# Kernel optimization log

Measured on AMD Instinct MI355X. Metric: run time of the kernel, lower is better.

The kernel has to match this reference:

```python
import jax, jax.numpy as jnp
import numpy as np

H = 8  # pinyin_feature_size = embedding_dim = GRU hidden size
VOCAB = 27


def setup_inputs() -> dict:
    key = jax.random.key(0)
    ks = jax.random.split(key, 10)
    B, T = 131072, 24
    inputs = jax.random.randint(ks[0], (B, T), 0, VOCAB, dtype=jnp.int32)
    emb = jax.random.normal(ks[1], (VOCAB, H), dtype=jnp.float32)
    emb = emb.at[0].set(0.0)  # padding_idx=0
    s = 0.25  # ~ 1/sqrt(hidden) init scale like torch GRU
    w_ih1 = jax.random.normal(ks[2], (3 * H, H), dtype=jnp.float32) * s
    w_hh1 = jax.random.normal(ks[3], (3 * H, H), dtype=jnp.float32) * s
    b_ih1 = jax.random.normal(ks[4], (3 * H,), dtype=jnp.float32) * s
    b_hh1 = jax.random.normal(ks[5], (3 * H,), dtype=jnp.float32) * s
    w_ih2 = jax.random.normal(ks[6], (3 * H, H), dtype=jnp.float32) * s
    w_hh2 = jax.random.normal(ks[7], (3 * H, H), dtype=jnp.float32) * s
    b_ih2 = jax.random.normal(ks[8], (3 * H,), dtype=jnp.float32) * s
    b_hh2 = jax.random.normal(ks[9], (3 * H,), dtype=jnp.float32) * s
    return {"inputs": inputs, "emb": emb,
            "w_ih1": w_ih1, "w_hh1": w_hh1, "b_ih1": b_ih1, "b_hh1": b_hh1,
            "w_ih2": w_ih2, "w_hh2": w_hh2, "b_ih2": b_ih2, "b_hh2": b_hh2}


def _gru_layer(x_seq, w_ih, w_hh, b_ih, b_hh):
    # x_seq: [B, T, H_in] -> all hidden states [B, T, H], final h [B, H]
    B = x_seq.shape[0]
    # precompute input-side gates for all timesteps: [T, B, 3H]
    gi_all = jnp.einsum('bti,gi->tbg', x_seq, w_ih) + b_ih
    h0 = jnp.zeros((B, H), dtype=x_seq.dtype)

    def cell(h, gi):
        gh = h @ w_hh.T + b_hh  # [B, 3H]
        i_r, i_z, i_n = jnp.split(gi, 3, axis=-1)
        h_r, h_z, h_n = jnp.split(gh, 3, axis=-1)
        r = jax.nn.sigmoid(i_r + h_r)
        z = jax.nn.sigmoid(i_z + h_z)
        n = jnp.tanh(i_n + r * h_n)
        h_new = (1.0 - z) * n + z * h
        return h_new, h_new

    h_last, hs = jax.lax.scan(cell, h0, gi_all)
    return jnp.swapaxes(hs, 0, 1), h_last  # [B, T, H], [B, H]


def reference(inputs, emb, w_ih1, w_hh1, b_ih1, b_hh1,
              w_ih2, w_hh2, b_ih2, b_hh2):
    # padding_idx=0 => row 0 of the table is zero
    emb_eff = emb.at[0].set(0.0)
    x = emb_eff[inputs]  # [B, T, H]
    h1_seq, _ = _gru_layer(x, w_ih1, w_hh1, b_ih1, b_hh1)
    # dropout(0.15) between layers is inactive in eval mode
    _, h2_last = _gru_layer(h1_seq, w_ih2, w_hh2, b_ih2, b_hh2)
    return h2_last  # [B, H] == output[1][-1]
```

## Files before the change

kernel.cpp:

```cpp
#include <hip/hip_runtime.h>


typedef __fp16 h2f    __attribute__((ext_vector_type(2)));
typedef __fp16 half8  __attribute__((ext_vector_type(8)));
typedef float  f32x16 __attribute__((ext_vector_type(16)));

#define LOG2E 1.44269504088896f

__device__ __forceinline__ h2f pk2f(float a, float b) {
  return __builtin_amdgcn_cvt_pkrtz(a, b);
}

union H8U { half8 h; unsigned u[4]; h2f p[4]; };

__device__ __forceinline__ unsigned from_upper(unsigned x) {
  auto r = __builtin_amdgcn_permlane32_swap((int)x, (int)x, false, false);
  return (unsigned)r[1];
}

__global__ __launch_bounds__(256, 4) void gru2_mfma(
    const int* __restrict__ inputs,
    const float* __restrict__ emb,
    const float* __restrict__ w_ih1, const float* __restrict__ w_hh1,
    const float* __restrict__ b_ih1, const float* __restrict__ b_hh1,
    const float* __restrict__ w_ih2, const float* __restrict__ w_hh2,
    const float* __restrict__ b_ih2, const float* __restrict__ b_hh2,
    float* __restrict__ out)
{
  __shared__ float G1f[27 * 33];
  __shared__ int   TK[128 * 25];

  const int tid   = threadIdx.x;
  const int lane  = tid & 63;
  const int wid   = tid >> 6;
  const int half_ = lane >> 5;
  const int col   = lane & 31;

  for (int idx = tid; idx < 27 * 24; idx += 256) {
    const int tok = idx / 24, g = idx - tok * 24;
    const float s = (g < 16) ? -LOG2E : 2.f * LOG2E;
    float a = b_ih1[g] + ((g < 16) ? b_hh1[g] : 0.f);
    if (tok != 0) {
      #pragma unroll
      for (int j = 0; j < 8; ++j) a = fmaf(w_ih1[g * 8 + j], emb[tok * 8 + j], a);
    }
    G1f[tok * 33 + g] = s * a;
  }

  const long gbase = (long)blockIdx.x * (128 * 24);
  #pragma unroll
  for (int k = 0; k < 12; ++k) {
    const int i = tid + k * 256;
    TK[(i / 24) * 25 + (i % 24)] = inputs[gbase + i];
  }
  __syncthreads();

  const int sl = wid * 32 + col;
  unsigned pkw[4] = {0u, 0u, 0u, 0u};
  #pragma unroll
  for (int t = 0; t < 24; ++t)
    pkw[t / 6] |= ((unsigned)TK[sl * 25 + t]) << (5 * (t % 6));
  const unsigned pk0 = pkw[0], pk1 = pkw[1], pk2_ = pkw[2], pk3 = pkw[3];

  auto tok_at = [&](int t) -> unsigned {
    const unsigned pw = (t < 6) ? pk0 : (t < 12) ? pk1 : (t < 18) ? pk2_ : pk3;
    return (pw >> (5 * (t % 6))) & 31u;
  };

  auto loadW = [&](const float* w) -> half8 {
    H8U u;
    u.u[0] = u.u[1] = u.u[2] = u.u[3] = 0u;
    if (half_ == 0 && col < 24) {
      const float s = (col < 16) ? -LOG2E : 2.f * LOG2E;
      const float4* p = (const float4*)(w + col * 8);
      const float4 x = p[0], y = p[1];
      u.p[0] = pk2f(x.x * s, x.y * s);
      u.p[1] = pk2f(x.z * s, x.w * s);
      u.p[2] = pk2f(y.x * s, y.y * s);
      u.p[3] = pk2f(y.z * s, y.w * s);
    }
    return u.h;
  };
  const half8 wa1  = loadW(w_hh1);
  const half8 wa2i = loadW(w_ih2);
  const half8 wa2h = loadW(w_hh2);

  f32x16 c2;
  #pragma unroll
  for (int r = 0; r < 16; ++r) {
    const int m = (r & 3) + 8 * (r >> 2) + 4 * half_;
    float v;
    if (m < 16)      v = -LOG2E * (b_ih2[m] + b_hh2[m]);
    else if (m < 24) v = 2.f * LOG2E * b_hh2[m];
    else             v = 0.f;
    c2[r] = v;
  }
  float bn1[4], bi2n[4];
  #pragma unroll
  for (int i = 0; i < 4; ++i) {
    bn1[i]  = 2.f * LOG2E * b_hh1[16 + 4 * half_ + i];
    bi2n[i] = 2.f * LOG2E * b_ih2[16 + 4 * half_ + i];
  }

  float h1v[4] = {0.f, 0.f, 0.f, 0.f}, h2v[4] = {0.f, 0.f, 0.f, 0.f};
  H8U f1, f2;
  f1.u[0] = f1.u[1] = f1.u[2] = f1.u[3] = 0u;
  f2 = f1;

  const float* g1base = G1f + half_ * 4;

  f32x16 c1;
  c1[8] = bn1[0]; c1[9] = bn1[1]; c1[10] = bn1[2]; c1[11] = bn1[3];
  c1[12] = 0.f; c1[13] = 0.f; c1[14] = 0.f; c1[15] = 0.f;
  float gin1[4];
  {
    const float* gp = g1base + tok_at(0) * 33;
    c1[0] = gp[0];  c1[1] = gp[1];  c1[2] = gp[2];  c1[3] = gp[3];
    c1[4] = gp[8];  c1[5] = gp[9];  c1[6] = gp[10]; c1[7] = gp[11];
    gin1[0] = gp[16]; gin1[1] = gp[17]; gin1[2] = gp[18]; gin1[3] = gp[19];
  }
  f32x16 d1 = c1;

  #pragma unroll
  for (int t = 0; t < 24; ++t) {
    float nc[8], ng[4];
    if (t < 23) {
      const float* gp = g1base + tok_at(t + 1) * 33;
      nc[0] = gp[0];  nc[1] = gp[1];  nc[2] = gp[2];  nc[3] = gp[3];
      nc[4] = gp[8];  nc[5] = gp[9];  nc[6] = gp[10]; nc[7] = gp[11];
      ng[0] = gp[16]; ng[1] = gp[17]; ng[2] = gp[18]; ng[3] = gp[19];
    }

    const f32x16 dh = __builtin_amdgcn_mfma_f32_32x32x16_f16(wa2h, f2.h, c2, 0, 0, 0);

    #pragma unroll
    for (int i = 0; i < 4; ++i) {
      const float r = __builtin_amdgcn_rcpf(1.f + __builtin_amdgcn_exp2f(d1[i]));
      const float z = __builtin_amdgcn_rcpf(1.f + __builtin_amdgcn_exp2f(d1[4 + i]));
      const float na = fmaf(r, d1[8 + i], gin1[i]);
      const float n = fmaf(-2.f, __builtin_amdgcn_rcpf(1.f + __builtin_amdgcn_exp2f(na)), 1.f);
      h1v[i] = n + z * (h1v[i] - n);
    }
    {
      const unsigned a = __builtin_bit_cast(unsigned, pk2f(h1v[0], h1v[1]));
      const unsigned b = __builtin_bit_cast(unsigned, pk2f(h1v[2], h1v[3]));
      f1.u[0] = a; f1.u[1] = b;
      f1.u[2] = from_upper(a); f1.u[3] = from_upper(b);
    }

    const f32x16 dg = __builtin_amdgcn_mfma_f32_32x32x16_f16(wa2i, f1.h, dh, 0, 0, 0);

    if (t < 23) {
      c1[0] = nc[0]; c1[1] = nc[1]; c1[2] = nc[2]; c1[3] = nc[3];
      c1[4] = nc[4]; c1[5] = nc[5]; c1[6] = nc[6]; c1[7] = nc[7];
      gin1[0] = ng[0]; gin1[1] = ng[1]; gin1[2] = ng[2]; gin1[3] = ng[3];
      d1 = __builtin_amdgcn_mfma_f32_32x32x16_f16(wa1, f1.h, c1, 0, 0, 0);
    }

    #pragma unroll
    for (int i = 0; i < 4; ++i) {
      const float r = __builtin_amdgcn_rcpf(1.f + __builtin_amdgcn_exp2f(dg[i]));
      const float z = __builtin_amdgcn_rcpf(1.f + __builtin_amdgcn_exp2f(dg[4 + i]));
      const float gin = dg[8 + i] - dh[8 + i] + bi2n[i];
      const float na = fmaf(r, dh[8 + i], gin);
      const float n = fmaf(-2.f, __builtin_amdgcn_rcpf(1.f + __builtin_amdgcn_exp2f(na)), 1.f);
      h2v[i] = n + z * (h2v[i] - n);
    }
    {
      const unsigned a = __builtin_bit_cast(unsigned, pk2f(h2v[0], h2v[1]));
      const unsigned b = __builtin_bit_cast(unsigned, pk2f(h2v[2], h2v[3]));
      f2.u[0] = a; f2.u[1] = b;
      f2.u[2] = from_upper(a); f2.u[3] = from_upper(b);
    }
  }

  const long seq = (long)blockIdx.x * 128 + sl;
  *(float4*)(out + seq * 8 + 4 * half_) =
      make_float4(h2v[0], h2v[1], h2v[2], h2v[3]);
}

extern "C" void kernel_launch(void* const* d_in, const int* in_sizes, int n_in,
                              void* d_out, int out_size, void* d_ws, size_t ws_size,
                              hipStream_t stream) {
  const int*   inputs = (const int*)d_in[0];
  const float* emb    = (const float*)d_in[1];
  const float* w_ih1  = (const float*)d_in[2];
  const float* w_hh1  = (const float*)d_in[3];
  const float* b_ih1  = (const float*)d_in[4];
  const float* b_hh1  = (const float*)d_in[5];
  const float* w_ih2  = (const float*)d_in[6];
  const float* w_hh2  = (const float*)d_in[7];
  const float* b_ih2  = (const float*)d_in[8];
  const float* b_hh2  = (const float*)d_in[9];
  float* out = (float*)d_out;

  const int B = in_sizes[0] / 24;
  const int grid = B / 128;

  hipLaunchKernelGGL(gru2_mfma, dim3(grid), dim3(256), 0, stream,
                     inputs, emb, w_ih1, w_hh1, b_ih1, b_hh1,
                     w_ih2, w_hh2, b_ih2, b_hh2, out);
}
```

Before: 112.2 us.

## Interleave two independent sequence groups per wave to hide MFMA latency

Each wave now processes two independent 32-sequence groups (A and B) and interleaves their MFMA and gate computations, so one group's math can fill the other's dependency stalls. Blocks cover 256 sequences, giving half as many blocks, and launch bounds drop to 2 blocks per CU to allow more registers. The old software prefetch of the next timestep's layer-1 gate inputs is removed, and these are now loaded from LDS within the same step. This trades occupancy and register pressure for instruction-level parallelism inside each wave.

```diff
diff --git a/kernel.cpp b/kernel.cpp
--- a/kernel.cpp
+++ b/kernel.cpp
@@ -18,7 +18,50 @@
   return (unsigned)r[1];
 }
 
-__global__ __launch_bounds__(256, 4) void gru2_mfma(
+#define MFMA_(A, B, C) __builtin_amdgcn_mfma_f32_32x32x16_f16((A), (B), (C), 0, 0, 0)
+
+#define TOKSEL(p0, p1, p2, p3, t) \
+  (((((t) < 6) ? (p0) : ((t) < 12) ? (p1) : ((t) < 18) ? (p2) : (p3)) >> (5 * ((t) % 6))) & 31u)
+
+#define BUILD_C1(c1, gp) do { \
+  (c1)[0] = (gp)[0];  (c1)[1] = (gp)[1];  (c1)[2] = (gp)[2];  (c1)[3] = (gp)[3]; \
+  (c1)[4] = (gp)[8];  (c1)[5] = (gp)[9];  (c1)[6] = (gp)[10]; (c1)[7] = (gp)[11]; \
+  (c1)[8] = bn1[0];  (c1)[9] = bn1[1];  (c1)[10] = bn1[2]; (c1)[11] = bn1[3]; \
+  (c1)[12] = 0.f; (c1)[13] = 0.f; (c1)[14] = 0.f; (c1)[15] = 0.f; \
+} while (0)
+
+#define L1_CELL(d1, gp, h1v, f1) do { \
+  _Pragma("unroll") \
+  for (int i = 0; i < 4; ++i) { \
+    const float r_ = __builtin_amdgcn_rcpf(1.f + __builtin_amdgcn_exp2f((d1)[i])); \
+    const float z_ = __builtin_amdgcn_rcpf(1.f + __builtin_amdgcn_exp2f((d1)[4 + i])); \
+    const float na_ = fmaf(r_, (d1)[8 + i], (gp)[16 + i]); \
+    const float n_ = fmaf(-2.f, __builtin_amdgcn_rcpf(1.f + __builtin_amdgcn_exp2f(na_)), 1.f); \
+    (h1v)[i] = n_ + z_ * ((h1v)[i] - n_); \
+  } \
+  const unsigned a_ = __builtin_bit_cast(unsigned, pk2f((h1v)[0], (h1v)[1])); \
+  const unsigned b_ = __builtin_bit_cast(unsigned, pk2f((h1v)[2], (h1v)[3])); \
+  (f1).u[0] = a_; (f1).u[1] = b_; \
+  (f1).u[2] = from_upper(a_); (f1).u[3] = from_upper(b_); \
+} while (0)
+
+#define L2_CELL(dg, dh, h2v, f2) do { \
+  _Pragma("unroll") \
+  for (int i = 0; i < 4; ++i) { \
+    const float r_ = __builtin_amdgcn_rcpf(1.f + __builtin_amdgcn_exp2f((dg)[i])); \
+    const float z_ = __builtin_amdgcn_rcpf(1.f + __builtin_amdgcn_exp2f((dg)[4 + i])); \
+    const float gin_ = (dg)[8 + i] - (dh)[8 + i] + bi2n[i]; \
+    const float na_ = fmaf(r_, (dh)[8 + i], gin_); \
+    const float n_ = fmaf(-2.f, __builtin_amdgcn_rcpf(1.f + __builtin_amdgcn_exp2f(na_)), 1.f); \
+    (h2v)[i] = n_ + z_ * ((h2v)[i] - n_); \
+  } \
+  const unsigned a_ = __builtin_bit_cast(unsigned, pk2f((h2v)[0], (h2v)[1])); \
+  const unsigned b_ = __builtin_bit_cast(unsigned, pk2f((h2v)[2], (h2v)[3])); \
+  (f2).u[0] = a_; (f2).u[1] = b_; \
+  (f2).u[2] = from_upper(a_); (f2).u[3] = from_upper(b_); \
+} while (0)
+
+__global__ __launch_bounds__(256, 2) void gru2_mfma(
     const int* __restrict__ inputs,
     const float* __restrict__ emb,
     const float* __restrict__ w_ih1, const float* __restrict__ w_hh1,
@@ -28,7 +71,7 @@
     float* __restrict__ out)
 {
   __shared__ float G1f[27 * 33];
-  __shared__ int   TK[128 * 25];
+  __shared__ int   TK[256 * 25];
 
   const int tid   = threadIdx.x;
   const int lane  = tid & 63;
@@ -47,25 +90,25 @@
     G1f[tok * 33 + g] = s * a;
   }
 
-  const long gbase = (long)blockIdx.x * (128 * 24);
-  #pragma unroll
-  for (int k = 0; k < 12; ++k) {
+  const long gbase = (long)blockIdx.x * (256 * 24);
+  #pragma unroll
+  for (int k = 0; k < 24; ++k) {
     const int i = tid + k * 256;
     TK[(i / 24) * 25 + (i % 24)] = inputs[gbase + i];
   }
   __syncthreads();
 
-  const int sl = wid * 32 + col;
-  unsigned pkw[4] = {0u, 0u, 0u, 0u};
-  #pragma unroll
-  for (int t = 0; t < 24; ++t)
-    pkw[t / 6] |= ((unsigned)TK[sl * 25 + t]) << (5 * (t % 6));
-  const unsigned pk0 = pkw[0], pk1 = pkw[1], pk2_ = pkw[2], pk3 = pkw[3];
-
-  auto tok_at = [&](int t) -> unsigned {
-    const unsigned pw = (t < 6) ? pk0 : (t < 12) ? pk1 : (t < 18) ? pk2_ : pk3;
-    return (pw >> (5 * (t % 6))) & 31u;
-  };
+  const int slA = wid * 64 + col;
+  const int slB = slA + 32;
+
+  unsigned pwA[4] = {0u, 0u, 0u, 0u}, pwB[4] = {0u, 0u, 0u, 0u};
+  #pragma unroll
+  for (int t = 0; t < 24; ++t) {
+    pwA[t / 6] |= ((unsigned)TK[slA * 25 + t]) << (5 * (t % 6));
+    pwB[t / 6] |= ((unsigned)TK[slB * 25 + t]) << (5 * (t % 6));
+  }
+  const unsigned pA0 = pwA[0], pA1 = pwA[1], pA2 = pwA[2], pA3 = pwA[3];
+  const unsigned pB0 = pwB[0], pB1 = pwB[1], pB2 = pwB[2], pB3 = pwB[3];
 
   auto loadW = [&](const float* w) -> half8 {
     H8U u;
@@ -102,81 +145,45 @@
     bi2n[i] = 2.f * LOG2E * b_ih2[16 + 4 * half_ + i];
   }
 
-  float h1v[4] = {0.f, 0.f, 0.f, 0.f}, h2v[4] = {0.f, 0.f, 0.f, 0.f};
-  H8U f1, f2;
-  f1.u[0] = f1.u[1] = f1.u[2] = f1.u[3] = 0u;
-  f2 = f1;
+  float h1vA[4] = {0.f, 0.f, 0.f, 0.f}, h2vA[4] = {0.f, 0.f, 0.f, 0.f};
+  float h1vB[4] = {0.f, 0.f, 0.f, 0.f}, h2vB[4] = {0.f, 0.f, 0.f, 0.f};
+  H8U f1A, f2A, f1B, f2B;
+  f1A.u[0] = f1A.u[1] = f1A.u[2] = f1A.u[3] = 0u;
+  f2A = f1A; f1B = f1A; f2B = f1A;
 
   const float* g1base = G1f + half_ * 4;
 
-  f32x16 c1;
-  c1[8] = bn1[0]; c1[9] = bn1[1]; c1[10] = bn1[2]; c1[11] = bn1[3];
-  c1[12] = 0.f; c1[13] = 0.f; c1[14] = 0.f; c1[15] = 0.f;
-  float gin1[4];
-  {
-    const float* gp = g1base + tok_at(0) * 33;
-    c1[0] = gp[0];  c1[1] = gp[1];  c1[2] = gp[2];  c1[3] = gp[3];
-    c1[4] = gp[8];  c1[5] = gp[9];  c1[6] = gp[10]; c1[7] = gp[11];
-    gin1[0] = gp[16]; gin1[1] = gp[17]; gin1[2] = gp[18]; gin1[3] = gp[19];
-  }
-  f32x16 d1 = c1;
-
   #pragma unroll
   for (int t = 0; t < 24; ++t) {
-    float nc[8], ng[4];
-    if (t < 23) {
-      const float* gp = g1base + tok_at(t + 1) * 33;
-      nc[0] = gp[0];  nc[1] = gp[1];  nc[2] = gp[2];  nc[3] = gp[3];
-      nc[4] = gp[8];  nc[5] = gp[9];  nc[6] = gp[10]; nc[7] = gp[11];
-      ng[0] = gp[16]; ng[1] = gp[17]; ng[2] = gp[18]; ng[3] = gp[19];
-    }
-
-    const f32x16 dh = __builtin_amdgcn_mfma_f32_32x32x16_f16(wa2h, f2.h, c2, 0, 0, 0);
-
-    #pragma unroll
-    for (int i = 0; i < 4; ++i) {
-      const float r = __builtin_amdgcn_rcpf(1.f + __builtin_amdgcn_exp2f(d1[i]));
-      const float z = __builtin_amdgcn_rcpf(1.f + __builtin_amdgcn_exp2f(d1[4 + i]));
-      const float na = fmaf(r, d1[8 + i], gin1[i]);
-      const float n = fmaf(-2.f, __builtin_amdgcn_rcpf(1.f + __builtin_amdgcn_exp2f(na)), 1.f);
-      h1v[i] = n + z * (h1v[i] - n);
-    }
-    {
-      const unsigned a = __builtin_bit_cast(unsigned, pk2f(h1v[0], h1v[1]));
-      const unsigned b = __builtin_bit_cast(unsigned, pk2f(h1v[2], h1v[3]));
-      f1.u[0] = a; f1.u[1] = b;
-      f1.u[2] = from_upper(a); f1.u[3] = from_upper(b);
-    }
-
-    const f32x16 dg = __builtin_amdgcn_mfma_f32_32x32x16_f16(wa2i, f1.h, dh, 0, 0, 0);
-
-    if (t < 23) {
-      c1[0] = nc[0]; c1[1] = nc[1]; c1[2] = nc[2]; c1[3] = nc[3];
-      c1[4] = nc[4]; c1[5] = nc[5]; c1[6] = nc[6]; c1[7] = nc[7];
-      gin1[0] = ng[0]; gin1[1] = ng[1]; gin1[2] = ng[2]; gin1[3] = ng[3];
-      d1 = __builtin_amdgcn_mfma_f32_32x32x16_f16(wa1, f1.h, c1, 0, 0, 0);
-    }
-
-    #pragma unroll
-    for (int i = 0; i < 4; ++i) {
-      const float r = __builtin_amdgcn_rcpf(1.f + __builtin_amdgcn_exp2f(dg[i]));
-      const float z = __builtin_amdgcn_rcpf(1.f + __builtin_amdgcn_exp2f(dg[4 + i]));
-      const float gin = dg[8 + i] - dh[8 + i] + bi2n[i];
-      const float na = fmaf(r, dh[8 + i], gin);
-      const float n = fmaf(-2.f, __builtin_amdgcn_rcpf(1.f + __builtin_amdgcn_exp2f(na)), 1.f);
-      h2v[i] = n + z * (h2v[i] - n);
-    }
-    {
-      const unsigned a = __builtin_bit_cast(unsigned, pk2f(h2v[0], h2v[1]));
-      const unsigned b = __builtin_bit_cast(unsigned, pk2f(h2v[2], h2v[3]));
-      f2.u[0] = a; f2.u[1] = b;
-      f2.u[2] = from_upper(a); f2.u[3] = from_upper(b);
-    }
-  }
-
-  const long seq = (long)blockIdx.x * 128 + sl;
-  *(float4*)(out + seq * 8 + 4 * half_) =
-      make_float4(h2v[0], h2v[1], h2v[2], h2v[3]);
+    const unsigned tokA = TOKSEL(pA0, pA1, pA2, pA3, t);
+    const unsigned tokB = TOKSEL(pB0, pB1, pB2, pB3, t);
+    const float* gpA = g1base + tokA * 33;
+    const float* gpB = g1base + tokB * 33;
+
+    f32x16 c1A, c1B;
+    BUILD_C1(c1A, gpA);
+    BUILD_C1(c1B, gpB);
+
+    const f32x16 dhA = MFMA_(wa2h, f2A.h, c2);
+    const f32x16 dhB = MFMA_(wa2h, f2B.h, c2);
+    const f32x16 d1A = MFMA_(wa1, f1A.h, c1A);
+    const f32x16 d1B = MFMA_(wa1, f1B.h, c1B);
+
+    L1_CELL(d1A, gpA, h1vA, f1A);
+    L1_CELL(d1B, gpB, h1vB, f1B);
+
+    const f32x16 dgA = MFMA_(wa2i, f1A.h, dhA);
+    const f32x16 dgB = MFMA_(wa2i, f1B.h, dhB);
+
+    L2_CELL(dgA, dhA, h2vA, f2A);
+    L2_CELL(dgB, dhB, h2vB, f2B);
+  }
+
+  const long base = (long)blockIdx.x * 256;
+  *(float4*)(out + (base + slA) * 8 + 4 * half_) =
+      make_float4(h2vA[0], h2vA[1], h2vA[2], h2vA[3]);
+  *(float4*)(out + (base + slB) * 8 + 4 * half_) =
+      make_float4(h2vB[0], h2vB[1], h2vB[2], h2vB[3]);
 }
 
 extern "C" void kernel_launch(void* const* d_in, const int* in_sizes, int n_in,
@@ -195,7 +202,7 @@
   float* out = (float*)d_out;
 
   const int B = in_sizes[0] / 24;
-  const int grid = B / 128;
+  const int grid = B / 256;
 
   hipLaunchKernelGGL(gru2_mfma, dim3(grid), dim3(256), 0, stream,
                      inputs, emb, w_ih1, w_hh1, b_ih1, b_hh1,
```

After: 116.5 us. 1.04x slower.
